# Kernel tuning notes

Hardware: AMD Instinct MI355X
Metric: run time of the kernel (lower is better)

Reference implementation:

```python
import jax, jax.numpy as jnp
import numpy as np

N_NODES = 100000
N_EDGES = 3200000
N_FEATS = 512
HIDDEN = 256
N_CLASSES = 64
K_STEPS = 10
ALPHA = 0.1


def setup_inputs() -> dict:
    key = jax.random.key(0)
    k1, k2, k3, k4 = jax.random.split(key, 4)
    x = jax.random.normal(k1, (N_NODES, N_FEATS), dtype=jnp.float32)
    edge_index = jax.random.randint(k2, (2, N_EDGES), 0, N_NODES, dtype=jnp.int64)
    W1 = jax.random.normal(k3, (N_FEATS, HIDDEN), dtype=jnp.float32) * (1.0 / np.sqrt(N_FEATS))
    b1 = jnp.zeros((HIDDEN,), dtype=jnp.float32)
    W2 = jax.random.normal(k4, (HIDDEN, N_CLASSES), dtype=jnp.float32) * (1.0 / np.sqrt(HIDDEN))
    b2 = jnp.zeros((N_CLASSES,), dtype=jnp.float32)
    return {"x": x, "edge_index": edge_index, "W1": W1, "b1": b1, "W2": W2, "b2": b2}


def reference(x, edge_index, W1, b1, W2, b2):
    # MLP (dropout is identity in eval mode)
    h = jax.nn.relu(x @ W1 + b1)            # [N, hidden]
    h = h @ W2 + b2                          # [N, C]

    # gcn_norm with self-loops: A_hat = D^{-1/2} (A + I) D^{-1/2}
    loop = jnp.arange(N_NODES, dtype=edge_index.dtype)
    src = jnp.concatenate([edge_index[0], loop])  # message source
    dst = jnp.concatenate([edge_index[1], loop])  # aggregation target
    ones = jnp.ones_like(dst, dtype=h.dtype)
    deg = jax.ops.segment_sum(ones, dst, num_segments=N_NODES)
    dinv = jnp.where(deg > 0, jax.lax.rsqrt(jnp.maximum(deg, 1.0)), 0.0)
    norm = dinv[src] * dinv[dst]             # [E+N]

    # APPNP: h_{t+1} = (1-alpha) * A_hat h_t + alpha * h_0
    h0 = h
    def step(hc, _):
        msg = norm[:, None] * hc[src]                       # gather + scale
        agg = jax.ops.segment_sum(msg, dst, num_segments=N_NODES)  # scatter-add
        return (1.0 - ALPHA) * agg + ALPHA * h0, None
    h, _ = jax.lax.scan(step, h, None, length=K_STEPS)

    return jax.nn.log_softmax(h, axis=1)
```

## Files before the change

### kernel.cpp

```cpp
#include <hip/hip_runtime.h>
#include <math.h>

#define NN 100000
#define NE 3200000
#define NF 512
#define NH 256
#define NC 64
#define KSTEPS 10
#define NB 391
#define CAP 96
#define NPH 8
#define FBP 1024

typedef _Float16 half8 __attribute__((ext_vector_type(8)));
typedef _Float16 h4v  __attribute__((ext_vector_type(4)));
typedef _Float16 h8v  __attribute__((ext_vector_type(8)));
typedef float f32x4 __attribute__((ext_vector_type(4)));


__global__ __launch_bounds__(256) void init_k(int* cnt, _Float16* y0, _Float16* yA, _Float16* yB) {
  int i = blockIdx.x * 256 + threadIdx.x;
  if (i < NN) cnt[i] = 0;
  if (blockIdx.x == 0) {
    int t = threadIdx.x;
    if (t < 64)       y0[(size_t)NN * NC + t] = (_Float16)0.f;
    else if (t < 128) yA[(size_t)NN * NC + (t - 64)] = (_Float16)0.f;
    else if (t < 192) yB[(size_t)NN * NC + (t - 128)] = (_Float16)0.f;
  }
}


__global__ __launch_bounds__(256) void fill_k(const int* __restrict__ dstI, const int* __restrict__ srcI,
                                              int* __restrict__ cnt, int* __restrict__ slots) {
  int ph = blockIdx.x & 7;
  int bi = blockIdx.x >> 3;
  int lo = ph * (NN / NPH);
  int hi = lo + (NN / NPH);
  for (int e = bi * 256 + threadIdx.x; e < NE; e += FBP * 256) {
    int d = __builtin_nontemporal_load(&dstI[e]);
    if (d >= lo && d < hi) {
      int s = __builtin_nontemporal_load(&srcI[e]);
      int pos = atomicAdd(&cnt[d], 1);
      if (pos < CAP) slots[(size_t)d * CAP + pos] = s;
    }
  }
}

__global__ __launch_bounds__(256) void pad_k(const int* __restrict__ cnt, int* __restrict__ slots) {
  int d = blockIdx.x * 256 + threadIdx.x;
  if (d >= NN) return;
  int c = cnt[d];
  int e = (c + 15) & ~15;
  for (int p = c; p < e; ++p) slots[(size_t)d * CAP + p] = NN;
}

__global__ __launch_bounds__(256) void dinv_k(const int* __restrict__ cnt, float* dinv, float* dsqrt, float* amul) {
  int i = blockIdx.x * 256 + threadIdx.x;
  if (i < NN) {
    float d = (float)(cnt[i] + 1);
    dinv[i]  = rsqrtf(d);
    dsqrt[i] = sqrtf(d);
    amul[i]  = 0.9f / d;
  }
}


__global__ __launch_bounds__(256) void cvtW1T_k(const float* __restrict__ W1, _Float16* __restrict__ W1T) {
  int t = blockIdx.x * 256 + threadIdx.x;
  int n = t >> 9, k = t & 511;
  W1T[t] = (_Float16)W1[k * NH + n];
}

__global__ __launch_bounds__(256) void cvtW2T_k(const float* __restrict__ W2, _Float16* __restrict__ W2T) {
  int t = blockIdx.x * 256 + threadIdx.x;
  int n = t >> 8, k = t & 255;
  W2T[t] = (_Float16)W2[k * NC + n];
}


__global__ __launch_bounds__(256) void mlp_k(const float* __restrict__ x, const _Float16* __restrict__ W1T,
                                             const float* __restrict__ b1, const _Float16* __restrict__ W2T,
                                             const float* __restrict__ b2, const float* __restrict__ dinv,
                                             _Float16* __restrict__ y0, _Float16* __restrict__ c0) {
  __shared__ _Float16 smem[16896];
  _Float16* As = smem;
  _Float16* Bs = smem + 64 * 40;
  _Float16* Hs = smem;

  const int t    = threadIdx.x;
  const int wave = t >> 6;
  const int lane = t & 63;
  const int l15  = lane & 15;
  const int q    = lane >> 4;
  const int m0   = blockIdx.x * 64;

  f32x4 acc[4][4] = {};

  for (int kk = 0; kk < NF; kk += 32) {
    __syncthreads();
    {
      int row = t >> 2;
      int kq  = (t & 3) << 3;
      int gr  = m0 + row;
      float4 v0 = make_float4(0.f, 0.f, 0.f, 0.f), v1 = v0;
      if (gr < NN) {
        const float* xp = &x[(size_t)gr * NF + kk + kq];
        v0 = *(const float4*)xp;
        v1 = *(const float4*)(xp + 4);
      }
      half8 hv;
      hv[0] = (_Float16)v0.x; hv[1] = (_Float16)v0.y; hv[2] = (_Float16)v0.z; hv[3] = (_Float16)v0.w;
      hv[4] = (_Float16)v1.x; hv[5] = (_Float16)v1.y; hv[6] = (_Float16)v1.z; hv[7] = (_Float16)v1.w;
      *(half8*)&As[row * 40 + kq] = hv;
    }
    #pragma unroll
    for (int i = 0; i < 4; ++i) {
      int idx = t + (i << 8);
      int n   = idx >> 2;
      int kq  = (idx & 3) << 3;
      *(half8*)&Bs[n * 40 + kq] = *(const half8*)&W1T[(size_t)n * NF + kk + kq];
    }
    __syncthreads();
    half8 af[4], bf[4];
    #pragma unroll
    for (int mi = 0; mi < 4; ++mi) af[mi] = *(half8*)&As[(mi * 16 + l15) * 40 + q * 8];
    #pragma unroll
    for (int ni = 0; ni < 4; ++ni) bf[ni] = *(half8*)&Bs[(wave * 64 + ni * 16 + l15) * 40 + q * 8];
    #pragma unroll
    for (int mi = 0; mi < 4; ++mi)
      #pragma unroll
      for (int ni = 0; ni < 4; ++ni)
        acc[mi][ni] = __builtin_amdgcn_mfma_f32_16x16x32_f16(af[mi], bf[ni], acc[mi][ni], 0, 0, 0);
  }
  __syncthreads();

  #pragma unroll
  for (int mi = 0; mi < 4; ++mi) {
    #pragma unroll
    for (int ni = 0; ni < 4; ++ni) {
      int ch = wave * 64 + ni * 16 + l15;
      float bb = b1[ch];
      #pragma unroll
      for (int r = 0; r < 4; ++r) {
        int m = mi * 16 + q * 4 + r;
        float v = acc[mi][ni][r] + bb;
        Hs[m * 264 + ch] = (_Float16)(v > 0.f ? v : 0.f);
      }
    }
  }
  __syncthreads();

  f32x4 acc2[4] = {};
  for (int kt = 0; kt < 8; ++kt) {
    half8 bf2 = *(const half8*)&W2T[(size_t)(wave * 16 + l15) * NH + kt * 32 + q * 8];
    #pragma unroll
    for (int mi = 0; mi < 4; ++mi) {
      half8 af2 = *(half8*)&Hs[(mi * 16 + l15) * 264 + kt * 32 + q * 8];
      acc2[mi] = __builtin_amdgcn_mfma_f32_16x16x32_f16(af2, bf2, acc2[mi], 0, 0, 0);
    }
  }
  int c = wave * 16 + l15;
  float bb2 = b2[c];
  #pragma unroll
  for (int mi = 0; mi < 4; ++mi)
    #pragma unroll
    for (int r = 0; r < 4; ++r) {
      int m = m0 + mi * 16 + q * 4 + r;
      if (m < NN) {
        float hv = acc2[mi][r] + bb2;
        float dv = dinv[m];
        y0[(size_t)m * NC + c] = (_Float16)(dv * hv);
        c0[(size_t)m * NC + c] = (_Float16)(0.1f * dv * hv);
      }
    }
}


__global__ __launch_bounds__(256) void appnp_k(const _Float16* __restrict__ y_in, const _Float16* __restrict__ c0,
                                               _Float16* __restrict__ y_out,
                                               const int* __restrict__ cnt, const int* __restrict__ slots,
                                               const float* __restrict__ amul) {
  const int lane = threadIdx.x & 63;
  const int g    = lane >> 3;
  const int fc   = lane & 7;
  int node = blockIdx.x * 4 + (threadIdx.x >> 6);
  node = __builtin_amdgcn_readfirstlane(node);
  const int pcnt = (cnt[node] + 15) & ~15;
  const int* row = slots + (size_t)node * CAP;
  const char* yb = (const char*)y_in;
  const unsigned foff = (unsigned)fc * 16u;

  h8v acc = { (_Float16)0.f, (_Float16)0.f, (_Float16)0.f, (_Float16)0.f,
              (_Float16)0.f, (_Float16)0.f, (_Float16)0.f, (_Float16)0.f };
  for (int e = 0; e < pcnt; e += 16) {
    #pragma unroll
    for (int j = 0; j < 2; ++j) {
      int idx = row[e + j * 8 + g];
      unsigned off = (unsigned)idx * 128u + foff;
      acc += *(const h8v*)(yb + off);
    }
  }

  #pragma unroll
  for (int d = 8; d <= 32; d <<= 1) {
    int4 ai = *(int4*)&acc;
    int4 o;
    o.x = __shfl_xor(ai.x, d, 64);
    o.y = __shfl_xor(ai.y, d, 64);
    o.z = __shfl_xor(ai.z, d, 64);
    o.w = __shfl_xor(ai.w, d, 64);
    acc += *(h8v*)&o;
  }

  if (g == 0) {
    size_t rowb = (size_t)node * 128 + foff;
    h8v self = *(const h8v*)((const char*)y_in + rowb);
    h8v cc   = *(const h8v*)((const char*)c0   + rowb);
    float am = amul[node];
    h8v r;
    #pragma unroll
    for (int i = 0; i < 8; ++i)
      r[i] = (_Float16)(am * ((float)acc[i] + (float)self[i]) + (float)cc[i]);
    *(h8v*)((char*)y_out + rowb) = r;
  }
}


__global__ __launch_bounds__(256) void lsm_k(const _Float16* __restrict__ y, const float* __restrict__ dsqrt,
                                             float* __restrict__ out) {
  int lane = threadIdx.x & 63;
  int node = blockIdx.x * 4 + (threadIdx.x >> 6);
  node = __builtin_amdgcn_readfirstlane(node);
  float v = (float)y[(size_t)node * NC + lane] * dsqrt[node];
  float m = v;
  #pragma unroll
  for (int off = 32; off > 0; off >>= 1) m = fmaxf(m, __shfl_xor(m, off, 64));
  float e = expf(v - m);
  float s = e;
  #pragma unroll
  for (int off = 32; off > 0; off >>= 1) s += __shfl_xor(s, off, 64);
  out[(size_t)node * NC + lane] = (v - m) - logf(s);
}


extern "C" void kernel_launch(void* const* d_in, const int* in_sizes, int n_in,
                              void* d_out, int out_size, void* d_ws, size_t ws_size,
                              hipStream_t stream) {
  (void)in_sizes; (void)n_in; (void)out_size; (void)ws_size;
  const float* x  = (const float*)d_in[0];
  const int*   ei = (const int*)d_in[1];
  const float* W1 = (const float*)d_in[2];
  const float* b1 = (const float*)d_in[3];
  const float* W2 = (const float*)d_in[4];
  const float* b2 = (const float*)d_in[5];
  float* out = (float*)d_out;

  const int* srcI = ei;
  const int* dstI = ei + NE;

  char* p = (char*)d_ws;
  auto carve = [&](size_t bytes) -> void* {
    void* q = (void*)p;
    p += (bytes + 255) & ~(size_t)255;
    return q;
  };
  _Float16* y0   = (_Float16*)carve((size_t)(NN + 1) * NC * 2);
  _Float16* yA   = (_Float16*)carve((size_t)(NN + 1) * NC * 2);
  _Float16* yB   = (_Float16*)carve((size_t)(NN + 1) * NC * 2);
  _Float16* c0   = (_Float16*)carve((size_t)NN * NC * 2);
  _Float16* W1T  = (_Float16*)carve((size_t)NH * NF * 2);
  _Float16* W2T  = (_Float16*)carve((size_t)NC * NH * 2);
  float* dinv    = (float*)carve((size_t)NN * 4);
  float* dsqrt   = (float*)carve((size_t)NN * 4);
  float* amul    = (float*)carve((size_t)NN * 4);
  int*   cnt     = (int*)carve((size_t)NN * 4);
  int*   slots   = (int*)carve((size_t)NN * CAP * 4);

  init_k   <<<NB, 256, 0, stream>>>(cnt, y0, yA, yB);
  fill_k   <<<NPH * FBP, 256, 0, stream>>>(dstI, srcI, cnt, slots);
  pad_k    <<<NB, 256, 0, stream>>>(cnt, slots);
  dinv_k   <<<NB, 256, 0, stream>>>(cnt, dinv, dsqrt, amul);
  cvtW1T_k <<<(NH * NF) / 256, 256, 0, stream>>>(W1, W1T);
  cvtW2T_k <<<(NC * NH) / 256, 256, 0, stream>>>(W2, W2T);
  mlp_k    <<<(NN + 63) / 64, 256, 0, stream>>>(x, W1T, b1, W2T, b2, dinv, y0, c0);

  const _Float16* yin = y0;
  _Float16* bufs[2] = { yA, yB };
  for (int it = 0; it < KSTEPS; ++it) {
    _Float16* yo = bufs[it & 1];
    appnp_k<<<NN / 4, 256, 0, stream>>>(yin, c0, yo, cnt, slots, amul);
    yin = yo;
  }
  lsm_k<<<NN / 4, 256, 0, stream>>>(yin, dsqrt, out);
}
```

Measured before the change: 1.037 ms.

## Replace multi-pass CSR fill with a two-stage shared-memory binning scatter

The edge fill used to scan the full destination array eight times, once per destination-range phase, and apply random atomics on each pass. It now makes one pass that bins packed (dst,src) pairs into 49 destination-range buckets using per-block shared-memory staging and batched global cursor atomics. A second kernel then walks each bucket and fills the per-node slots, giving each XCD-striped block set a local address range. The bucket storage reuses the not-yet-used yA/yB/c0 feature buffers, and the zeroing of padding rows moves into dinv_k so it runs after that reuse. This cuts repeated index reads and scattered traffic, but it adds an extra write and read of the pairs and relies on fixed bucket capacities.

```diff
diff --git a/kernel.cpp b/kernel.cpp
--- a/kernel.cpp
+++ b/kernel.cpp
@@ -9,37 +9,90 @@
 #define KSTEPS 10
 #define NB 391
 #define CAP 96
-#define NPH 8
-#define FBP 1024
+
+#define NBUK 49
+#define BSH 11
+#define BCAP 70000
+#define BUF 64
+#define BINB 1024
+#define PER 3125
+#define FITER 8
 
 typedef _Float16 half8 __attribute__((ext_vector_type(8)));
 typedef _Float16 h4v  __attribute__((ext_vector_type(4)));
 typedef _Float16 h8v  __attribute__((ext_vector_type(8)));
 typedef float f32x4 __attribute__((ext_vector_type(4)));
 
-
-__global__ __launch_bounds__(256) void init_k(int* cnt, _Float16* y0, _Float16* yA, _Float16* yB) {
+static __device__ __forceinline__ long long packDS(int d, int s) {
+  return (long long)(((unsigned long long)(unsigned)s << 32) | (unsigned)d);
+}
+
+
+__global__ __launch_bounds__(256) void init_k(int* cnt, int* cursor) {
   int i = blockIdx.x * 256 + threadIdx.x;
   if (i < NN) cnt[i] = 0;
-  if (blockIdx.x == 0) {
-    int t = threadIdx.x;
-    if (t < 64)       y0[(size_t)NN * NC + t] = (_Float16)0.f;
-    else if (t < 128) yA[(size_t)NN * NC + (t - 64)] = (_Float16)0.f;
-    else if (t < 192) yB[(size_t)NN * NC + (t - 128)] = (_Float16)0.f;
-  }
-}
-
-
-__global__ __launch_bounds__(256) void fill_k(const int* __restrict__ dstI, const int* __restrict__ srcI,
-                                              int* __restrict__ cnt, int* __restrict__ slots) {
-  int ph = blockIdx.x & 7;
-  int bi = blockIdx.x >> 3;
-  int lo = ph * (NN / NPH);
-  int hi = lo + (NN / NPH);
-  for (int e = bi * 256 + threadIdx.x; e < NE; e += FBP * 256) {
-    int d = __builtin_nontemporal_load(&dstI[e]);
-    if (d >= lo && d < hi) {
-      int s = __builtin_nontemporal_load(&srcI[e]);
+  if (blockIdx.x == 0 && threadIdx.x < NBUK) cursor[threadIdx.x] = 0;
+}
+
+
+__global__ __launch_bounds__(256) void bin_k(const int* __restrict__ dstI, const int* __restrict__ srcI,
+                                             int* __restrict__ cursor, long long* __restrict__ bucket) {
+  __shared__ long long buf[NBUK][BUF];
+  __shared__ int bcnt[NBUK];
+  const int t    = threadIdx.x;
+  const int wave = t >> 6;
+  const int lane = t & 63;
+  if (t < NBUK) bcnt[t] = 0;
+  __syncthreads();
+
+  int eBeg = blockIdx.x * PER;
+  int eEnd = eBeg + PER; if (eEnd > NE) eEnd = NE;
+
+  for (int base = eBeg; base < eEnd; base += 256 * FITER) {
+    #pragma unroll
+    for (int it = 0; it < FITER; ++it) {
+      int e = base + it * 256 + t;
+      if (e < eEnd) {
+        int d = __builtin_nontemporal_load(&dstI[e]);
+        int s = __builtin_nontemporal_load(&srcI[e]);
+        int b = d >> BSH;
+        int pos = atomicAdd(&bcnt[b], 1);
+        if (pos < BUF) {
+          buf[b][pos] = packDS(d, s);
+        } else {
+          int g = atomicAdd(&cursor[b], 1);
+          if (g < BCAP) bucket[(size_t)b * BCAP + g] = packDS(d, s);
+        }
+      }
+    }
+    __syncthreads();
+    for (int b = wave; b < NBUK; b += 4) {
+      int n = bcnt[b]; if (n > BUF) n = BUF;
+      int g = 0;
+      if (lane == 0 && n > 0) g = atomicAdd(&cursor[b], n);
+      g = __shfl(g, 0, 64);
+      if (lane < n) {
+        int gi = g + lane;
+        if (gi < BCAP) bucket[(size_t)b * BCAP + gi] = buf[b][lane];
+      }
+      if (lane == 0) bcnt[b] = 0;
+    }
+    __syncthreads();
+  }
+}
+
+
+__global__ __launch_bounds__(256) void scatter_k(const long long* __restrict__ bucket, const int* __restrict__ cursor,
+                                                 int* __restrict__ cnt, int* __restrict__ slots) {
+  int xcd = blockIdx.x & 7;
+  int ks  = blockIdx.x >> 3;
+  for (int b = xcd; b < NBUK; b += 8) {
+    int n = cursor[b]; if (n > BCAP) n = BCAP;
+    const long long* bp = bucket + (size_t)b * BCAP;
+    for (int i = ks * 256 + threadIdx.x; i < n; i += 256 * 256) {
+      long long v = __builtin_nontemporal_load(&bp[i]);
+      int d = (int)(unsigned)(v & 0xffffffffll);
+      int s = (int)(unsigned)((unsigned long long)v >> 32);
       int pos = atomicAdd(&cnt[d], 1);
       if (pos < CAP) slots[(size_t)d * CAP + pos] = s;
     }
@@ -54,13 +107,20 @@
   for (int p = c; p < e; ++p) slots[(size_t)d * CAP + p] = NN;
 }
 
-__global__ __launch_bounds__(256) void dinv_k(const int* __restrict__ cnt, float* dinv, float* dsqrt, float* amul) {
+__global__ __launch_bounds__(256) void dinv_k(const int* __restrict__ cnt, float* dinv, float* dsqrt, float* amul,
+                                              _Float16* y0, _Float16* yA, _Float16* yB) {
   int i = blockIdx.x * 256 + threadIdx.x;
   if (i < NN) {
     float d = (float)(cnt[i] + 1);
     dinv[i]  = rsqrtf(d);
     dsqrt[i] = sqrtf(d);
     amul[i]  = 0.9f / d;
+  }
+  if (blockIdx.x == 0) {
+    int t = threadIdx.x;
+    if (t < 64)       y0[(size_t)NN * NC + t] = (_Float16)0.f;
+    else if (t < 128) yA[(size_t)NN * NC + (t - 64)] = (_Float16)0.f;
+    else if (t < 192) yB[(size_t)NN * NC + (t - 128)] = (_Float16)0.f;
   }
 }
 
@@ -275,11 +335,15 @@
   float* amul    = (float*)carve((size_t)NN * 4);
   int*   cnt     = (int*)carve((size_t)NN * 4);
   int*   slots   = (int*)carve((size_t)NN * CAP * 4);
-
-  init_k   <<<NB, 256, 0, stream>>>(cnt, y0, yA, yB);
-  fill_k   <<<NPH * FBP, 256, 0, stream>>>(dstI, srcI, cnt, slots);
+  int*   cursor  = (int*)carve((size_t)NBUK * 4);
+
+  long long* bucket = (long long*)yA;
+
+  init_k   <<<NB, 256, 0, stream>>>(cnt, cursor);
+  bin_k    <<<BINB, 256, 0, stream>>>(dstI, srcI, cursor, bucket);
+  scatter_k<<<2048, 256, 0, stream>>>(bucket, cursor, cnt, slots);
   pad_k    <<<NB, 256, 0, stream>>>(cnt, slots);
-  dinv_k   <<<NB, 256, 0, stream>>>(cnt, dinv, dsqrt, amul);
+  dinv_k   <<<NB, 256, 0, stream>>>(cnt, dinv, dsqrt, amul, y0, yA, yB);
   cvtW1T_k <<<(NH * NF) / 256, 256, 0, stream>>>(W1, W1T);
   cvtW2T_k <<<(NC * NH) / 256, 256, 0, stream>>>(W2, W2T);
   mlp_k    <<<(NN + 63) / 64, 256, 0, stream>>>(x, W1T, b1, W2T, b2, dinv, y0, c0);
```

After: 1.881 ms. +81.5%, slower.
